# Performance work log

Hardware: AMD Instinct MI355X
Metric: run time of the kernel (lower is better)

## Reference

```python
import jax, jax.numpy as jnp
import numpy as np


def setup_inputs() -> dict:
    key = jax.random.key(0)
    k0, k1, k2, k3, k4 = jax.random.split(key, 5)
    T, B, S, H = 32, 8192, 256, 128
    return {
        "states_batch": jax.random.normal(k0, (T, B, S), dtype=jnp.float32),
        "W1": jax.random.normal(k1, (T, S, H), dtype=jnp.float32) * (S ** -0.5),
        "b1": jax.random.normal(k2, (T, H), dtype=jnp.float32) * 0.01,
        "W2": jax.random.normal(k3, (T, H, 1), dtype=jnp.float32) * 0.01,
        "b2": jax.random.normal(k4, (T, 1), dtype=jnp.float32) * 0.01,
    }


def reference(states_batch, W1, b1, W2, b2):
    # [T,B,S] @ [T,S,H] -> [T,B,H], bias, SiLU
    h = jnp.einsum('tbs,tsh->tbh', states_batch, W1) + b1[:, None, :]
    h = jax.nn.silu(h)
    # [T,B,H] @ [T,H,1] -> [T,B,1], bias, squeeze -> [T,B]
    out = jnp.einsum('tbh,tho->tbo', h, W2) + b2[:, None, :]
    return out.squeeze(-1)
```

## Files before the change

### kernel.cpp

```cpp
#include <hip/hip_runtime.h>
#include <hip/hip_bf16.h>

typedef __attribute__((ext_vector_type(8))) short bf16x8;
typedef __attribute__((ext_vector_type(4))) float f32x4;

#define T_DIM 32
#define B_DIM 8192
#define S_DIM 256
#define H_DIM 128
#define NCH   8
#define BLOCKS_PER_T 16

__device__ __forceinline__ uint32_t cvt_pk_bf16(float lo, float hi) {
  uint32_t r;
  asm("v_cvt_pk_bf16_f32 %0, %1, %2" : "=v"(r) : "v"(lo), "v"(hi));
  return r;
}

#define ISSUE(av, c)                                                           \
  _Pragma("unroll")                                                            \
  for (int ks = 0; ks < 8; ++ks) {                                             \
    av[ks * 2]     = A4[(c) * 1024 + l15 * 64 + ks * 8 + lg * 2];              \
    av[ks * 2 + 1] = A4[(c) * 1024 + l15 * 64 + ks * 8 + lg * 2 + 1];          \
  }

#define COMPUTE(av, c)                                                         \
  {                                                                            \
    f32x4 acc[8];                                                              \
    _Pragma("unroll")                                                          \
    for (int nt = 0; nt < 8; ++nt) acc[nt] = (f32x4){0.f, 0.f, 0.f, 0.f};      \
    _Pragma("unroll")                                                          \
    for (int ks = 0; ks < 8; ++ks) {                                           \
      union { uint32_t u[4]; bf16x8 v; } uu;                                   \
      uu.u[0] = cvt_pk_bf16(av[ks * 2].x,     av[ks * 2].y);                   \
      uu.u[1] = cvt_pk_bf16(av[ks * 2].z,     av[ks * 2].w);                   \
      uu.u[2] = cvt_pk_bf16(av[ks * 2 + 1].x, av[ks * 2 + 1].y);               \
      uu.u[3] = cvt_pk_bf16(av[ks * 2 + 1].z, av[ks * 2 + 1].w);               \
      _Pragma("unroll")                                                        \
      for (int nt = 0; nt < 8; ++nt) {                                         \
        const bf16x8 bq = *reinterpret_cast<const bf16x8*>(                    \
            &ldsW[((nt * 8 + ks) * 64 + lane) * 16]);                          \
        acc[nt] = __builtin_amdgcn_mfma_f32_16x16x32_bf16(uu.v, bq,            \
                                                          acc[nt], 0, 0, 0);  \
      }                                                                        \
    }                                                                          \
    float part[4];                                                             \
    _Pragma("unroll")                                                          \
    for (int r = 0; r < 4; ++r) {                                              \
      float s = 0.f;                                                           \
      _Pragma("unroll")                                                        \
      for (int nt = 0; nt < 8; ++nt) {                                         \
        const float h   = acc[nt][r] + b1c[nt];                                \
        const float sig = 1.f / (1.f + __expf(-h));                            \
        s += h * sig * w2c[nt];                                                \
      }                                                                        \
      s += __shfl_xor(s, 1);                                                   \
      s += __shfl_xor(s, 2);                                                   \
      s += __shfl_xor(s, 4);                                                   \
      s += __shfl_xor(s, 8);                                                   \
      part[r] = s;                                                             \
    }                                                                          \
    if (l15 == 0) {                                                            \
      f32x4 o = {part[0] + b2t, part[1] + b2t, part[2] + b2t, part[3] + b2t};  \
      *reinterpret_cast<f32x4*>(&outw[(c) * 16 + lg * 4]) = o;                 \
    }                                                                          \
  }

__global__ __launch_bounds__(256, 2) void cvar_mlp_kernel(
    const float* __restrict__ states, const float* __restrict__ W1,
    const float* __restrict__ b1, const float* __restrict__ W2,
    const float* __restrict__ b2, float* __restrict__ out)
{
  __shared__ __align__(16) char ldsW[64 * 1024];

  const int tid  = threadIdx.x;
  const int wid  = tid >> 6;
  const int lane = tid & 63;
  const int l15  = lane & 15;
  const int lg   = lane >> 4;

  const int bidx = blockIdx.x;
  const int xcd  = bidx & 7;
  const int slot = bidx >> 3;
  const int t    = xcd * 4 + (slot >> 4);
  const int cg   = slot & 15;

  const float*  Aw = states + ((size_t)t * B_DIM + cg * 512 + wid * 128) * S_DIM;
  const float4* A4 = reinterpret_cast<const float4*>(Aw);
  float*       outw = out + (size_t)t * B_DIM + cg * 512 + wid * 128;

  float4 avA[16], avB[16];
  ISSUE(avA, 0);

  const float* W1g = W1 + (size_t)t * (S_DIM * H_DIM);
#pragma unroll
  for (int p = 0; p < 2; ++p) {
    const int nt   = wid * 2 + p;
    const int ncol = nt * 16 + l15;
#pragma unroll
    for (int ks = 0; ks < 8; ++ks) {
      const int kbase = ks * 32 + lg * 8;
      float e[8];
#pragma unroll
      for (int j = 0; j < 8; ++j)
        e[j] = W1g[(size_t)(kbase + j) * H_DIM + ncol];
      union { uint32_t u[4]; bf16x8 v; } uu;
      uu.u[0] = cvt_pk_bf16(e[0], e[1]);
      uu.u[1] = cvt_pk_bf16(e[2], e[3]);
      uu.u[2] = cvt_pk_bf16(e[4], e[5]);
      uu.u[3] = cvt_pk_bf16(e[6], e[7]);
      *reinterpret_cast<bf16x8*>(&ldsW[((nt * 8 + ks) * 64 + lane) * 16]) = uu.v;
    }
  }

  float b1c[8], w2c[8];
#pragma unroll
  for (int nt = 0; nt < 8; ++nt) {
    const int col = nt * 16 + l15;
    b1c[nt] = b1[(size_t)t * H_DIM + col];
    w2c[nt] = W2[(size_t)t * H_DIM + col];
  }
  const float b2t = b2[t];

  __syncthreads();

#pragma unroll 1
  for (int c = 0; c < NCH; c += 2) {
    ISSUE(avB, c + 1);
    COMPUTE(avA, c);
    if (c + 2 < NCH) { ISSUE(avA, c + 2); }
    COMPUTE(avB, c + 1);
  }
}

extern "C" void kernel_launch(void* const* d_in, const int* in_sizes, int n_in,
                              void* d_out, int out_size, void* d_ws, size_t ws_size,
                              hipStream_t stream) {
  const float* states = (const float*)d_in[0];
  const float* W1     = (const float*)d_in[1];
  const float* b1     = (const float*)d_in[2];
  const float* W2     = (const float*)d_in[3];
  const float* b2     = (const float*)d_in[4];
  float* out          = (float*)d_out;

  const int grid = T_DIM * BLOCKS_PER_T;
  cvar_mlp_kernel<<<grid, 256, 0, stream>>>(states, W1, b1, W2, b2, out);
}
```

Before: 57.93 us.

## Stage activation tiles in swizzled LDS and keep W1 fragments in registers

The kernel moves from a per-wave 128-row slice with all of W1 staged in LDS to a block-cooperative scheme. All 256 threads load 32-row activation chunks with coalesced nontemporal loads, convert them to bf16 and write them into double-buffered XOR-swizzled LDS. Each wave keeps only its 32-column slice of W1 in registers, and partial outputs are reduced across the four waves through shared memory. This cuts LDS traffic for B operands and improves global load coalescing, at the cost of two barriers per chunk and a cross-wave reduction.

New measurement: 65.57 us. 13.2% more time.

```diff
diff --git a/kernel.cpp b/kernel.cpp
--- a/kernel.cpp
+++ b/kernel.cpp
@@ -8,7 +8,8 @@
 #define B_DIM 8192
 #define S_DIM 256
 #define H_DIM 128
-#define NCH   8
+#define BM    32
+#define NCH   16
 #define BLOCKS_PER_T 16
 
 __device__ __forceinline__ uint32_t cvt_pk_bf16(float lo, float hi) {
@@ -17,53 +18,82 @@
   return r;
 }
 
-#define ISSUE(av, c)                                                           \
+#define BARRIER() asm volatile("s_waitcnt lgkmcnt(0)\n\ts_barrier" ::: "memory")
+
+#define ISSUE8(av, c)                                                          \
   _Pragma("unroll")                                                            \
-  for (int ks = 0; ks < 8; ++ks) {                                             \
-    av[ks * 2]     = A4[(c) * 1024 + l15 * 64 + ks * 8 + lg * 2];              \
-    av[ks * 2 + 1] = A4[(c) * 1024 + l15 * 64 + ks * 8 + lg * 2 + 1];          \
+  for (int j = 0; j < 8; ++j)                                                  \
+    av[j] = __builtin_nontemporal_load(&A4[(size_t)(c) * 2048 + j * 256 + tid]);
+
+#define CONVERT8(av, LDSBUF)                                                   \
+  _Pragma("unroll")                                                            \
+  for (int j = 0; j < 8; ++j) {                                                \
+    const int f   = j * 256 + tid;                                             \
+    const int row = f >> 6;                                                    \
+    const int kq  = f & 63;                                                    \
+    const uint32_t lo = cvt_pk_bf16(av[j].x, av[j].y);                         \
+    const uint32_t hi = cvt_pk_bf16(av[j].z, av[j].w);                         \
+    const int byteoff = (row * 512 + kq * 8) ^ ((row & 7) << 4);               \
+    *reinterpret_cast<uint2*>(&(LDSBUF)[byteoff]) = make_uint2(lo, hi);        \
   }
 
-#define COMPUTE(av, c)                                                         \
+#define MFMA_EPI(LDSBUF, RI)                                                   \
   {                                                                            \
-    f32x4 acc[8];                                                              \
+    f32x4 acc[2][2];                                                           \
     _Pragma("unroll")                                                          \
-    for (int nt = 0; nt < 8; ++nt) acc[nt] = (f32x4){0.f, 0.f, 0.f, 0.f};      \
+    for (int mt = 0; mt < 2; ++mt) {                                           \
+      acc[mt][0] = (f32x4){0.f, 0.f, 0.f, 0.f};                                \
+      acc[mt][1] = (f32x4){0.f, 0.f, 0.f, 0.f};                                \
+    }                                                                          \
     _Pragma("unroll")                                                          \
-    for (int ks = 0; ks < 8; ++ks) {                                           \
-      union { uint32_t u[4]; bf16x8 v; } uu;                                   \
-      uu.u[0] = cvt_pk_bf16(av[ks * 2].x,     av[ks * 2].y);                   \
-      uu.u[1] = cvt_pk_bf16(av[ks * 2].z,     av[ks * 2].w);                   \
-      uu.u[2] = cvt_pk_bf16(av[ks * 2 + 1].x, av[ks * 2 + 1].y);               \
-      uu.u[3] = cvt_pk_bf16(av[ks * 2 + 1].z, av[ks * 2 + 1].w);               \
+    for (int mt = 0; mt < 2; ++mt) {                                           \
+      const int row = mt * 16 + l15;                                           \
+      bf16x8 afr[8];                                                           \
       _Pragma("unroll")                                                        \
-      for (int nt = 0; nt < 8; ++nt) {                                         \
-        const bf16x8 bq = *reinterpret_cast<const bf16x8*>(                    \
-            &ldsW[((nt * 8 + ks) * 64 + lane) * 16]);                          \
-        acc[nt] = __builtin_amdgcn_mfma_f32_16x16x32_bf16(uu.v, bq,            \
-                                                          acc[nt], 0, 0, 0);  \
+      for (int ks = 0; ks < 8; ++ks) {                                         \
+        const int byteoff =                                                    \
+            (row * 512 + ks * 64 + lg * 16) ^ ((row & 7) << 4);                \
+        afr[ks] = *reinterpret_cast<const bf16x8*>(&(LDSBUF)[byteoff]);        \
+      }                                                                        \
+      _Pragma("unroll")                                                        \
+      for (int ks = 0; ks < 8; ++ks) {                                         \
+        acc[mt][0] = __builtin_amdgcn_mfma_f32_16x16x32_bf16(                  \
+            afr[ks], bfr[0][ks], acc[mt][0], 0, 0, 0);                         \
+        acc[mt][1] = __builtin_amdgcn_mfma_f32_16x16x32_bf16(                  \
+            afr[ks], bfr[1][ks], acc[mt][1], 0, 0, 0);                         \
       }                                                                        \
     }                                                                          \
-    float part[4];                                                             \
     _Pragma("unroll")                                                          \
-    for (int r = 0; r < 4; ++r) {                                              \
-      float s = 0.f;                                                           \
+    for (int mt = 0; mt < 2; ++mt) {                                           \
+      float part[4];                                                           \
       _Pragma("unroll")                                                        \
-      for (int nt = 0; nt < 8; ++nt) {                                         \
-        const float h   = acc[nt][r] + b1c[nt];                                \
-        const float sig = 1.f / (1.f + __expf(-h));                            \
-        s += h * sig * w2c[nt];                                                \
+      for (int r = 0; r < 4; ++r) {                                            \
+        float s = 0.f;                                                         \
+        _Pragma("unroll")                                                      \
+        for (int nloc = 0; nloc < 2; ++nloc) {                                 \
+          const float h   = acc[mt][nloc][r] + b1c[nloc];                      \
+          const float sig = 1.f / (1.f + __expf(-h));                          \
+          s += h * sig * w2c[nloc];                                            \
+        }                                                                      \
+        s += __shfl_xor(s, 1);                                                 \
+        s += __shfl_xor(s, 2);                                                 \
+        s += __shfl_xor(s, 4);                                                 \
+        s += __shfl_xor(s, 8);                                                 \
+        part[r] = s;                                                           \
       }                                                                        \
-      s += __shfl_xor(s, 1);                                                   \
-      s += __shfl_xor(s, 2);                                                   \
-      s += __shfl_xor(s, 4);                                                   \
-      s += __shfl_xor(s, 8);                                                   \
-      part[r] = s;                                                             \
+      if (l15 == 0) {                                                          \
+        _Pragma("unroll")                                                      \
+        for (int r = 0; r < 4; ++r)                                            \
+          red[RI][wid][mt * 16 + lg * 4 + r] = part[r];                        \
+      }                                                                        \
     }                                                                          \
-    if (l15 == 0) {                                                            \
-      f32x4 o = {part[0] + b2t, part[1] + b2t, part[2] + b2t, part[3] + b2t};  \
-      *reinterpret_cast<f32x4*>(&outw[(c) * 16 + lg * 4]) = o;                 \
-    }                                                                          \
+  }
+
+#define OUTW(RI, cc)                                                           \
+  if (tid < BM) {                                                              \
+    const float o = red[RI][0][tid] + red[RI][1][tid] + red[RI][2][tid] +      \
+                    red[RI][3][tid] + b2t;                                     \
+    __builtin_nontemporal_store(o, &outw[(cc) * BM + tid]);                    \
   }
 
 __global__ __launch_bounds__(256, 2) void cvar_mlp_kernel(
@@ -71,7 +101,8 @@
     const float* __restrict__ b1, const float* __restrict__ W2,
     const float* __restrict__ b2, float* __restrict__ out)
 {
-  __shared__ __align__(16) char ldsW[64 * 1024];
+  __shared__ __align__(16) char ldsA[2][BM * 512];
+  __shared__ float red[2][4][BM];
 
   const int tid  = threadIdx.x;
   const int wid  = tid >> 6;
@@ -84,19 +115,21 @@
   const int slot = bidx >> 3;
   const int t    = xcd * 4 + (slot >> 4);
   const int cg   = slot & 15;
+  const int b0   = cg * (BM * NCH);
 
-  const float*  Aw = states + ((size_t)t * B_DIM + cg * 512 + wid * 128) * S_DIM;
-  const float4* A4 = reinterpret_cast<const float4*>(Aw);
-  float*       outw = out + (size_t)t * B_DIM + cg * 512 + wid * 128;
+  const float* Ag  = states + ((size_t)t * B_DIM + b0) * S_DIM;
+  const f32x4* A4  = reinterpret_cast<const f32x4*>(Ag);
+  const float* W1g = W1 + (size_t)t * (S_DIM * H_DIM);
+  float*      outw = out + (size_t)t * B_DIM + b0;
 
-  float4 avA[16], avB[16];
-  ISSUE(avA, 0);
+  f32x4 avA[8], avB[8];
+  ISSUE8(avA, 0);
+  ISSUE8(avB, 1);
 
-  const float* W1g = W1 + (size_t)t * (S_DIM * H_DIM);
+  bf16x8 bfr[2][8];
 #pragma unroll
-  for (int p = 0; p < 2; ++p) {
-    const int nt   = wid * 2 + p;
-    const int ncol = nt * 16 + l15;
+  for (int nloc = 0; nloc < 2; ++nloc) {
+    const int ncol = (wid * 2 + nloc) * 16 + l15;
 #pragma unroll
     for (int ks = 0; ks < 8; ++ks) {
       const int kbase = ks * 32 + lg * 8;
@@ -109,27 +142,40 @@
       uu.u[1] = cvt_pk_bf16(e[2], e[3]);
       uu.u[2] = cvt_pk_bf16(e[4], e[5]);
       uu.u[3] = cvt_pk_bf16(e[6], e[7]);
-      *reinterpret_cast<bf16x8*>(&ldsW[((nt * 8 + ks) * 64 + lane) * 16]) = uu.v;
+      bfr[nloc][ks] = uu.v;
     }
   }
 
-  float b1c[8], w2c[8];
+  float b1c[2], w2c[2];
 #pragma unroll
-  for (int nt = 0; nt < 8; ++nt) {
-    const int col = nt * 16 + l15;
-    b1c[nt] = b1[(size_t)t * H_DIM + col];
-    w2c[nt] = W2[(size_t)t * H_DIM + col];
+  for (int nloc = 0; nloc < 2; ++nloc) {
+    const int col = (wid * 2 + nloc) * 16 + l15;
+    b1c[nloc] = b1[(size_t)t * H_DIM + col];
+    w2c[nloc] = W2[(size_t)t * H_DIM + col];
   }
   const float b2t = b2[t];
 
-  __syncthreads();
+  CONVERT8(avA, ldsA[0]);
+  ISSUE8(avA, 2);
+  BARRIER();
 
 #pragma unroll 1
   for (int c = 0; c < NCH; c += 2) {
-    ISSUE(avB, c + 1);
-    COMPUTE(avA, c);
-    if (c + 2 < NCH) { ISSUE(avA, c + 2); }
-    COMPUTE(avB, c + 1);
+    MFMA_EPI(ldsA[0], 0);
+    if (c + 1 < NCH) {
+      CONVERT8(avB, ldsA[1]);
+      if (c + 3 < NCH) ISSUE8(avB, c + 3);
+    }
+    BARRIER();
+    OUTW(0, c);
+
+    MFMA_EPI(ldsA[1], 1);
+    if (c + 2 < NCH) {
+      CONVERT8(avA, ldsA[0]);
+      if (c + 4 < NCH) ISSUE8(avA, c + 4);
+    }
+    BARRIER();
+    OUTW(1, c + 1);
   }
 }
 
```
